# Optimization experiments

Hardware: AMD Instinct MI355X
Metric: run time of the kernel (lower is better)

## Reference

```python
import jax, jax.numpy as jnp
import numpy as np

C = 256
NUM_HEADS = 8
EPS = 1e-5


def setup_inputs() -> dict:
    key = jax.random.key(0)
    ks = jax.random.split(key, 8)
    x = jax.random.normal(ks[0], (2, C, 64, 64), dtype=jnp.float32)
    # LayerNorm params (torch default: weight=1, bias=0)
    norm_w = jnp.ones((C,), jnp.float32)
    norm_b = jnp.zeros((C,), jnp.float32)
    # qkv Linear: weight (3C, C), bias (3C,)
    qkv_w = jax.random.normal(ks[1], (3 * C, C), dtype=jnp.float32) * (1.0 / np.sqrt(C))
    qkv_b = jax.random.normal(ks[2], (3 * C,), dtype=jnp.float32) * 0.01
    # proj Linear: weight (C, C), bias (C,)
    proj_w = jax.random.normal(ks[3], (C, C), dtype=jnp.float32) * (1.0 / np.sqrt(C))
    proj_b = jax.random.normal(ks[4], (C,), dtype=jnp.float32) * 0.01
    # gamma initialized to zeros in torch, but use small nonzero so output depends on attention
    gamma = jnp.full((1,), 0.1, jnp.float32)
    return {"x": x, "norm_w": norm_w, "norm_b": norm_b, "qkv_w": qkv_w,
            "qkv_b": qkv_b, "proj_w": proj_w, "proj_b": proj_b, "gamma": gamma}


def reference(x, norm_w, norm_b, qkv_w, qkv_b, proj_w, proj_b, gamma):
    B, Cc, H, W = x.shape
    N = H * W
    nh = NUM_HEADS
    hd = Cc // nh
    scale = hd ** (-0.5)

    # (B, N, C)
    x_flat = x.reshape(B, Cc, N).transpose(0, 2, 1)

    # LayerNorm over last dim
    mu = jnp.mean(x_flat, axis=-1, keepdims=True)
    var = jnp.mean(jnp.square(x_flat - mu), axis=-1, keepdims=True)
    x_norm = (x_flat - mu) * jax.lax.rsqrt(var + EPS) * norm_w + norm_b

    # QKV projection: (B, N, 3C) -> (3, B, nh, N, hd)
    qkv = x_norm @ qkv_w.T + qkv_b
    qkv = qkv.reshape(B, N, 3, nh, hd).transpose(2, 0, 3, 1, 4)
    q, k, v = qkv[0], qkv[1], qkv[2]

    # attention scores (B, nh, N, N); note torch code scales AFTER q@k.T
    attn = jnp.einsum('bhnd,bhmd->bhnm', q, k) * scale
    attn = jax.nn.softmax(attn, axis=-1)

    # (B, nh, N, hd) -> (B, N, C)
    x_attn = jnp.einsum('bhnm,bhmd->bhnd', attn, v)
    x_attn = x_attn.transpose(0, 2, 1, 3).reshape(B, N, Cc)
    x_attn = x_attn @ proj_w.T + proj_b

    # back to (B, C, H, W) and scaled residual
    x_attn = x_attn.transpose(0, 2, 1).reshape(B, Cc, H, W)
    return gamma * x_attn + x
```

## Files before the change

kernel.cpp:

```cpp
#include <hip/hip_runtime.h>

#define CCH   256
#define NSEQ  4096
#define NH    8
#define HD    32

typedef short s8x __attribute__((ext_vector_type(8)));
typedef float f4x __attribute__((ext_vector_type(4)));

__device__ __forceinline__ f4x mfma16(s8x a, s8x b, f4x c) {
  return __builtin_amdgcn_mfma_f32_16x16x32_bf16(a, b, c, 0, 0, 0);
}

__device__ __forceinline__ unsigned short f2bf(float f) {
  union { float f; unsigned int u; } v; v.f = f;
  unsigned int u = v.u + 0x7fffu + ((v.u >> 16) & 1u);
  return (unsigned short)(u >> 16);
}

__device__ __forceinline__ unsigned int pk_bf_rnd(float lo, float hi) {
  return (unsigned int)f2bf(lo) | ((unsigned int)f2bf(hi) << 16);
}

__device__ __forceinline__ unsigned int pk_bf_trunc(float lo, float hi) {
  union { float f; unsigned int u; } a, b; a.f = lo; b.f = hi;
  return __builtin_amdgcn_perm(b.u, a.u, 0x07060302);
}

#if defined(__has_builtin)
#if __has_builtin(__builtin_amdgcn_exp2f)
#define FEXP2(x) __builtin_amdgcn_exp2f(x)
#endif
#endif
#ifndef FEXP2
__device__ __forceinline__ float __fexp2_asm(float x) {
  float r; asm("v_exp_f32 %0, %1" : "=v"(r) : "v"(x)); return r;
}
#define FEXP2(x) __fexp2_asm(x)
#endif

#define C2SCALE (0.17677669529663689f * 1.4426950408889634f)

__global__ __launch_bounds__(256) void ln_cvt_kernel(const float* __restrict__ x,
                                                     const float* __restrict__ nw,
                                                     const float* __restrict__ nb,
                                                     unsigned short* __restrict__ xn,
                                                     const float* __restrict__ qw,
                                                     const float* __restrict__ pw,
                                                     unsigned short* __restrict__ qwb,
                                                     unsigned short* __restrict__ pwb) {
  if (blockIdx.x >= 256) {
    const int t = (blockIdx.x - 256) * 256 + threadIdx.x;
    const float4* src;
    unsigned short* dst;
    int idx;
    if (t < 49152) { src = reinterpret_cast<const float4*>(qw); dst = qwb; idx = t; }
    else           { src = reinterpret_cast<const float4*>(pw); dst = pwb; idx = t - 49152; }
    const float4 vv = src[idx];
    union { unsigned short u[4]; uint2 v; } pk;
    pk.u[0] = f2bf(vv.x); pk.u[1] = f2bf(vv.y); pk.u[2] = f2bf(vv.z); pk.u[3] = f2bf(vv.w);
    *reinterpret_cast<uint2*>(dst + 4 * idx) = pk.v;
    return;
  }

  __shared__ float Ls[256 * 32];
  __shared__ float Sred[2][32][8];
  const int t  = threadIdx.x;
  const int n  = t & 31;
  const int cg = t >> 5;
  const int p0 = blockIdx.x * 32;
  const int b  = p0 >> 12;
  const int n0 = p0 & 4095;
  const float* xb = x + (size_t)b * CCH * NSEQ + n0;

  #pragma unroll
  for (int i = 0; i < 32; ++i) {
    const int c = i * 8 + cg;
    Ls[c * 32 + (n ^ (c & 31))] = xb[(size_t)c * NSEQ + n];
  }
  __syncthreads();

  float s = 0.f, sq = 0.f;
  #pragma unroll
  for (int j = 0; j < 32; ++j) {
    const int c = cg * 32 + j;
    const float v = Ls[c * 32 + (n ^ j)];
    s += v; sq += v * v;
  }
  Sred[0][n][cg] = s; Sred[1][n][cg] = sq;
  __syncthreads();
  float ts = 0.f, tq = 0.f;
  #pragma unroll
  for (int g = 0; g < 8; ++g) { ts += Sred[0][n][g]; tq += Sred[1][n][g]; }
  const float mean = ts * (1.f / 256.f);
  const float rstd = rsqrtf(tq * (1.f / 256.f) - mean * mean + 1e-5f);

  unsigned short* orow = xn + ((size_t)b * NSEQ + n0 + n) * CCH + cg * 32;
  #pragma unroll
  for (int j8 = 0; j8 < 4; ++j8) {
    unsigned int w_[4];
    #pragma unroll
    for (int hw = 0; hw < 4; ++hw) {
      const int j = j8 * 8 + hw * 2;
      const int c = cg * 32 + j;
      const float v0 = Ls[c * 32 + (n ^ j)];
      const float v1 = Ls[(c + 1) * 32 + (n ^ (j + 1))];
      const float y0 = (v0 - mean) * rstd * nw[c] + nb[c];
      const float y1 = (v1 - mean) * rstd * nw[c + 1] + nb[c + 1];
      w_[hw] = pk_bf_rnd(y0, y1);
    }
    uint4 pkv; pkv.x = w_[0]; pkv.y = w_[1]; pkv.z = w_[2]; pkv.w = w_[3];
    *reinterpret_cast<uint4*>(orow + j8 * 8) = pkv;
  }
}

#define GEMM_CORE(A_PTR, B_PTR, ACC)                                            \
  {                                                                             \
    for (int kb = 0; kb < 4; ++kb) {                                            \
      if (kb) __syncthreads();                                                  \
      _Pragma("unroll")                                                         \
      for (int j = 0; j < 4; ++j) {                                             \
        const int c = j * 256 + tid;                                            \
        const int ar = c >> 3, acr = c & 7;                                     \
        *reinterpret_cast<s8x*>(&As[ar * 64 + ((acr ^ (ar & 7)) << 3)]) =       \
          *reinterpret_cast<const s8x*>(A_PTR + (size_t)(mt * 128 + ar) * CCH + kb * 64 + acr * 8); \
      }                                                                         \
      _Pragma("unroll")                                                         \
      for (int j = 0; j < 2; ++j) {                                             \
        const int c = j * 256 + tid;                                            \
        const int br = c >> 3, bcr = c & 7;                                     \
        *reinterpret_cast<s8x*>(&Bs[br * 64 + ((bcr ^ (br & 7)) << 3)]) =       \
          *reinterpret_cast<const s8x*>(B_PTR + (size_t)(nt * 64 + br) * CCH + kb * 64 + bcr * 8); \
      }                                                                         \
      __syncthreads();                                                          \
      _Pragma("unroll")                                                         \
      for (int kin = 0; kin < 2; ++kin) {                                       \
        const int chx = ((kin * 4 + quad) ^ (l16 & 7)) << 3;                    \
        const s8x a0 = *reinterpret_cast<const s8x*>(&As[(wv * 32 + l16) * 64 + chx]);      \
        const s8x a1 = *reinterpret_cast<const s8x*>(&As[(wv * 32 + 16 + l16) * 64 + chx]); \
        _Pragma("unroll")                                                       \
        for (int ni = 0; ni < 4; ++ni) {                                        \
          const s8x bf = *reinterpret_cast<const s8x*>(&Bs[(ni * 16 + l16) * 64 + chx]);    \
          ACC[0][ni] = mfma16(a0, bf, ACC[0][ni]);                              \
          ACC[1][ni] = mfma16(a1, bf, ACC[1][ni]);                              \
        }                                                                       \
      }                                                                         \
    }                                                                           \
  }

__global__ __launch_bounds__(256, 3) void qkv_gemm(const unsigned short* __restrict__ xn,
                                                   const unsigned short* __restrict__ w,
                                                   const float* __restrict__ bias,
                                                   unsigned short* __restrict__ q,
                                                   unsigned short* __restrict__ k,
                                                   unsigned short* __restrict__ vt) {
  __shared__ unsigned short As[128 * 64];
  __shared__ unsigned short Bs[64 * 64];
  const int tid = threadIdx.x;
  const int wv  = tid >> 6;
  const int lane = tid & 63;
  const int quad = lane >> 4, l16 = lane & 15;
  const int mt = blockIdx.x;
  const int nt = blockIdx.y;

  f4x acc[2][4];
  #pragma unroll
  for (int mi = 0; mi < 2; ++mi)
    #pragma unroll
    for (int ni = 0; ni < 4; ++ni)
      acc[mi][ni] = (f4x){0.f, 0.f, 0.f, 0.f};

  GEMM_CORE(xn, w, acc)

  const int sel = nt >> 2;
  #pragma unroll
  for (int ni = 0; ni < 4; ++ni) {
    const int o = nt * 64 + ni * 16 + l16;
    const float bs = bias[o];
    const int ol = o & 255;
    const int head = ol >> 5, d = ol & 31;
    #pragma unroll
    for (int mi = 0; mi < 2; ++mi) {
      const int g0 = mt * 128 + wv * 32 + mi * 16 + quad * 4;
      const int bb = g0 >> 12, n0 = g0 & 4095;
      if (sel == 2) {
        unsigned short* vp = vt + ((size_t)(bb * NH + head) * HD + d) * NSEQ + n0;
        uint2 pk;
        pk.x = pk_bf_rnd(acc[mi][ni][0] + bs, acc[mi][ni][1] + bs);
        pk.y = pk_bf_rnd(acc[mi][ni][2] + bs, acc[mi][ni][3] + bs);
        *reinterpret_cast<uint2*>(vp) = pk;
      } else {
        const float sc = (sel == 0) ? C2SCALE : 1.f;
        unsigned short* base = (sel == 0) ? q : k;
        #pragma unroll
        for (int r = 0; r < 4; ++r)
          base[((size_t)(bb * NH + head) * NSEQ + n0 + r) * HD + d] = f2bf((acc[mi][ni][r] + bs) * sc);
      }
    }
  }
}

__global__ __launch_bounds__(256, 3) void proj_gemm(const unsigned short* __restrict__ xa,
                                                    const unsigned short* __restrict__ w,
                                                    const float* __restrict__ bias,
                                                    const float* __restrict__ gamma,
                                                    const float* __restrict__ x,
                                                    float* __restrict__ out) {
  __shared__ unsigned short As[128 * 64];
  __shared__ unsigned short Bs[64 * 64];
  const int tid = threadIdx.x;
  const int wv  = tid >> 6;
  const int lane = tid & 63;
  const int quad = lane >> 4, l16 = lane & 15;
  const int mt = blockIdx.x;
  const int nt = blockIdx.y;

  f4x acc[2][4];
  #pragma unroll
  for (int mi = 0; mi < 2; ++mi)
    #pragma unroll
    for (int ni = 0; ni < 4; ++ni)
      acc[mi][ni] = (f4x){0.f, 0.f, 0.f, 0.f};

  GEMM_CORE(xa, w, acc)

  const float g0 = gamma[0];
  #pragma unroll
  for (int ni = 0; ni < 4; ++ni) {
    const int c = nt * 64 + ni * 16 + l16;
    const float bs = bias[c];
    #pragma unroll
    for (int mi = 0; mi < 2; ++mi) {
      const int gr = mt * 128 + wv * 32 + mi * 16 + quad * 4;
      const int bb = gr >> 12, n0 = gr & 4095;
      const size_t off = (size_t)(bb * CCH + c) * NSEQ + n0;
      const float4 xv = *reinterpret_cast<const float4*>(x + off);
      float4 ov;
      ov.x = g0 * (acc[mi][ni][0] + bs) + xv.x;
      ov.y = g0 * (acc[mi][ni][1] + bs) + xv.y;
      ov.z = g0 * (acc[mi][ni][2] + bs) + xv.z;
      ov.w = g0 * (acc[mi][ni][3] + bs) + xv.w;
      *reinterpret_cast<float4*>(out + off) = ov;
    }
  }
}

__global__ __launch_bounds__(256, 4) void fa_kernel(const unsigned short* __restrict__ q,
                                                    const unsigned short* __restrict__ k,
                                                    const unsigned short* __restrict__ vt,
                                                    float* __restrict__ Opart,
                                                    float* __restrict__ Lpart) {
  __shared__ unsigned short Ks[2][64 * 40];
  __shared__ unsigned short Vs[2][32 * 72];
  __shared__ unsigned short Ps[128 * 72];

  const int tid  = threadIdx.x;
  const int wv   = tid >> 6;
  const int lane = tid & 63;
  const int quad = lane >> 4;
  const int l16  = lane & 15;
  const int i    = blockIdx.x;
  const int bh   = i & 15;
  const int rest = i >> 4;
  const int half = rest & 1;
  const int qblk = rest >> 1;
  const int kv0  = half * 2048;

  const unsigned short* kb_ = k  + ((size_t)bh * NSEQ + kv0) * HD;
  const unsigned short* vb_ = vt + (size_t)bh * HD * NSEQ + kv0;

  const int krow = tid >> 2;
  const int kdc  = (tid & 3) * 8;
  const int vrow = tid >> 3;
  const int vkc  = (tid & 7) * 8;

  s8x bq0, bq1;
  {
    const unsigned short* qb = q + ((size_t)bh * NSEQ + (size_t)qblk * 128 + wv * 32) * HD;
    bq0 = *reinterpret_cast<const s8x*>(qb + (size_t)l16 * HD + quad * 8);
    bq1 = *reinterpret_cast<const s8x*>(qb + (size_t)(16 + l16) * HD + quad * 8);
  }

  uint4 kreg = *reinterpret_cast<const uint4*>(kb_ + (size_t)krow * HD + kdc);
  uint4 vreg = *reinterpret_cast<const uint4*>(vb_ + (size_t)vrow * NSEQ + vkc);
  *reinterpret_cast<uint4*>(&Ks[0][krow * 40 + kdc]) = kreg;
  *reinterpret_cast<uint4*>(&Vs[0][vrow * 72 + vkc]) = vreg;
  kreg = *reinterpret_cast<const uint4*>(kb_ + (size_t)(64 + krow) * HD + kdc);
  vreg = *reinterpret_cast<const uint4*>(vb_ + (size_t)vrow * NSEQ + 64 + vkc);
  __syncthreads();

  f4x st[4][2];
  #pragma unroll
  for (int ii = 0; ii < 4; ++ii) {
    const s8x ak = *reinterpret_cast<const s8x*>(&Ks[0][(ii * 16 + l16) * 40 + quad * 8]);
    const f4x z = {0.f, 0.f, 0.f, 0.f};
    st[ii][0] = mfma16(ak, bq0, z);
    st[ii][1] = mfma16(ak, bq1, z);
  }

  f4x oacc[2][2];
  #pragma unroll
  for (int dt = 0; dt < 2; ++dt)
    #pragma unroll
    for (int ct = 0; ct < 2; ++ct)
      oacc[dt][ct] = (f4x){0.f, 0.f, 0.f, 0.f};
  f4x accL[2] = {(f4x){0.f, 0.f, 0.f, 0.f}, (f4x){0.f, 0.f, 0.f, 0.f}};

  s8x ones;
  #pragma unroll
  for (int j = 0; j < 8; ++j) ones[j] = (short)0x3F80;

  const int r0 = (wv * 32 + l16) * 72;
  const int r1 = (wv * 32 + 16 + l16) * 72;

  for (int t = 0; t < 32; ++t) {
    const int c = t & 1;

    if (t + 1 < 32) {
      *reinterpret_cast<uint4*>(&Ks[c ^ 1][krow * 40 + kdc]) = kreg;
      *reinterpret_cast<uint4*>(&Vs[c ^ 1][vrow * 72 + vkc]) = vreg;
    }

    #pragma unroll
    for (int ct = 0; ct < 2; ++ct) {
      const int prow = (wv * 32 + ct * 16 + l16) * 72;
      #pragma unroll
      for (int ii = 0; ii < 4; ++ii) {
        const float e0 = FEXP2(st[ii][ct][0]);
        const float e1 = FEXP2(st[ii][ct][1]);
        const float e2 = FEXP2(st[ii][ct][2]);
        const float e3 = FEXP2(st[ii][ct][3]);
        uint2 pw;
        pw.x = pk_bf_trunc(e0, e1);
        pw.y = pk_bf_trunc(e2, e3);
        *reinterpret_cast<uint2*>(&Ps[prow + ii * 16 + quad * 4]) = pw;
      }
    }

    if (t + 2 < 32) {
      kreg = *reinterpret_cast<const uint4*>(kb_ + (size_t)((t + 2) * 64 + krow) * HD + kdc);
      vreg = *reinterpret_cast<const uint4*>(vb_ + (size_t)vrow * NSEQ + (t + 2) * 64 + vkc);
    }

    #pragma unroll
    for (int kb2 = 0; kb2 < 2; ++kb2) {
      const s8x bp0 = *reinterpret_cast<const s8x*>(&Ps[r0 + kb2 * 32 + quad * 8]);
      const s8x bp1 = *reinterpret_cast<const s8x*>(&Ps[r1 + kb2 * 32 + quad * 8]);
      const s8x av0 = *reinterpret_cast<const s8x*>(&Vs[c][l16 * 72 + kb2 * 32 + quad * 8]);
      const s8x av1 = *reinterpret_cast<const s8x*>(&Vs[c][(16 + l16) * 72 + kb2 * 32 + quad * 8]);
      oacc[0][0] = mfma16(av0, bp0, oacc[0][0]);
      oacc[1][0] = mfma16(av1, bp0, oacc[1][0]);
      oacc[0][1] = mfma16(av0, bp1, oacc[0][1]);
      oacc[1][1] = mfma16(av1, bp1, oacc[1][1]);
      accL[0] = mfma16(ones, bp0, accL[0]);
      accL[1] = mfma16(ones, bp1, accL[1]);
    }

    __syncthreads();

    if (t + 1 < 32) {
      #pragma unroll
      for (int ii = 0; ii < 4; ++ii) {
        const s8x ak = *reinterpret_cast<const s8x*>(&Ks[c ^ 1][(ii * 16 + l16) * 40 + quad * 8]);
        const f4x z = {0.f, 0.f, 0.f, 0.f};
        st[ii][0] = mfma16(ak, bq0, z);
        st[ii][1] = mfma16(ak, bq1, z);
      }
    }
  }

  #pragma unroll
  for (int ct = 0; ct < 2; ++ct) {
    const int qg = qblk * 128 + wv * 32 + ct * 16 + l16;
    float* obase = Opart + ((size_t)(half * 16 + bh) * NSEQ + qg) * HD;
    #pragma unroll
    for (int dt = 0; dt < 2; ++dt) {
      float4 ov;
      ov.x = oacc[dt][ct][0]; ov.y = oacc[dt][ct][1];
      ov.z = oacc[dt][ct][2]; ov.w = oacc[dt][ct][3];
      *reinterpret_cast<float4*>(obase + dt * 16 + quad * 4) = ov;
    }
    if (quad == 0)
      Lpart[(size_t)(half * 16 + bh) * NSEQ + qg] = accL[ct][0];
  }
}

__global__ __launch_bounds__(256) void fa_combine(const float* __restrict__ Opart,
                                                  const float* __restrict__ Lpart,
                                                  unsigned short* __restrict__ xa) {
  const int t  = blockIdx.x * 256 + threadIdx.x;
  const int c8 = t & 3;
  const int n  = (t >> 2) & 4095;
  const int bh = t >> 14;
  const int b  = bh >> 3, h = bh & 7;

  const size_t o0 = ((size_t)bh * NSEQ + n) * HD + c8 * 8;
  const size_t o1 = o0 + (size_t)16 * NSEQ * HD;
  const float4 a0 = *reinterpret_cast<const float4*>(Opart + o0);
  const float4 a1 = *reinterpret_cast<const float4*>(Opart + o0 + 4);
  const float4 b0 = *reinterpret_cast<const float4*>(Opart + o1);
  const float4 b1 = *reinterpret_cast<const float4*>(Opart + o1 + 4);
  const float l0 = Lpart[(size_t)bh * NSEQ + n];
  const float l1 = Lpart[(size_t)(16 + bh) * NSEQ + n];
  const float rl = 1.f / (l0 + l1);

  uint4 ow;
  ow.x = pk_bf_rnd((a0.x + b0.x) * rl, (a0.y + b0.y) * rl);
  ow.y = pk_bf_rnd((a0.z + b0.z) * rl, (a0.w + b0.w) * rl);
  ow.z = pk_bf_rnd((a1.x + b1.x) * rl, (a1.y + b1.y) * rl);
  ow.w = pk_bf_rnd((a1.z + b1.z) * rl, (a1.w + b1.w) * rl);
  *reinterpret_cast<uint4*>(xa + ((size_t)b * NSEQ + n) * CCH + h * HD + c8 * 8) = ow;
}

extern "C" void kernel_launch(void* const* d_in, const int* in_sizes, int n_in,
                              void* d_out, int out_size, void* d_ws, size_t ws_size,
                              hipStream_t stream) {
  const float* x      = (const float*)d_in[0];
  const float* norm_w = (const float*)d_in[1];
  const float* norm_b = (const float*)d_in[2];
  const float* qkv_w  = (const float*)d_in[3];
  const float* qkv_b  = (const float*)d_in[4];
  const float* proj_w = (const float*)d_in[5];
  const float* proj_b = (const float*)d_in[6];
  const float* gamma  = (const float*)d_in[7];
  float* out = (float*)d_out;

  char* ws = (char*)d_ws;
  unsigned short* xn  = (unsigned short*)(ws);
  unsigned short* qwb = (unsigned short*)(ws + 4194304);
  unsigned short* pwb = (unsigned short*)(ws + 4587520);
  unsigned short* q   = (unsigned short*)(ws + 4718592);
  unsigned short* k   = (unsigned short*)(ws + 8912896);
  unsigned short* vt  = (unsigned short*)(ws + 13107200);
  unsigned short* xa  = (unsigned short*)(ws + 17301504);
  float* Opart        = (float*)(ws + 21495808);
  float* Lpart        = (float*)(ws + 38273024);

  hipLaunchKernelGGL(ln_cvt_kernel, dim3(512), dim3(256), 0, stream,
                     x, norm_w, norm_b, xn, qkv_w, proj_w, qwb, pwb);
  hipLaunchKernelGGL(qkv_gemm,  dim3(64, 12), dim3(256), 0, stream, xn, qwb, qkv_b, q, k, vt);
  hipLaunchKernelGGL(fa_kernel, dim3(1024), dim3(256), 0, stream, q, k, vt, Opart, Lpart);
  hipLaunchKernelGGL(fa_combine, dim3(1024), dim3(256), 0, stream, Opart, Lpart, xa);
  hipLaunchKernelGGL(proj_gemm, dim3(64, 4), dim3(256), 0, stream, xa, pwb, proj_b, gamma, x, out);
}
```

Measured before the change: 154.8 us.

## Load K/V straight into registers and software-pipeline PV with double-buffered P

Each wave now loads its K and V MFMA fragments directly from global memory into double-buffered registers, instead of staging them through shared memory. This removes the shared K/V tiles and the per-iteration __syncthreads. The P·V product is deferred by one iteration, using a double-buffered P tile in LDS that each wave owns privately, so the exp/pack work overlaps the MFMA work. In exchange, every wave re-reads the full K/V tile, which raises global and L2 traffic roughly fourfold, and register pressure rises enough that launch bounds drop from 4 to 3 blocks per CU.

```diff
diff --git a/kernel.cpp b/kernel.cpp
--- a/kernel.cpp
+++ b/kernel.cpp
@@ -245,14 +245,12 @@
   }
 }
 
-__global__ __launch_bounds__(256, 4) void fa_kernel(const unsigned short* __restrict__ q,
+__global__ __launch_bounds__(256, 3) void fa_kernel(const unsigned short* __restrict__ q,
                                                     const unsigned short* __restrict__ k,
                                                     const unsigned short* __restrict__ vt,
                                                     float* __restrict__ Opart,
                                                     float* __restrict__ Lpart) {
-  __shared__ unsigned short Ks[2][64 * 40];
-  __shared__ unsigned short Vs[2][32 * 72];
-  __shared__ unsigned short Ps[128 * 72];
+  __shared__ unsigned short Ps[2][128 * 72];
 
   const int tid  = threadIdx.x;
   const int wv   = tid >> 6;
@@ -269,10 +267,9 @@
   const unsigned short* kb_ = k  + ((size_t)bh * NSEQ + kv0) * HD;
   const unsigned short* vb_ = vt + (size_t)bh * HD * NSEQ + kv0;
 
-  const int krow = tid >> 2;
-  const int kdc  = (tid & 3) * 8;
-  const int vrow = tid >> 3;
-  const int vkc  = (tid & 7) * 8;
+  const unsigned short* kp  = kb_ + (size_t)l16 * HD + quad * 8;
+  const unsigned short* vpA = vb_ + (size_t)l16 * NSEQ + quad * 8;
+  const unsigned short* vpB = vb_ + (size_t)(16 + l16) * NSEQ + quad * 8;
 
   s8x bq0, bq1;
   {
@@ -281,21 +278,25 @@
     bq1 = *reinterpret_cast<const s8x*>(qb + (size_t)(16 + l16) * HD + quad * 8);
   }
 
-  uint4 kreg = *reinterpret_cast<const uint4*>(kb_ + (size_t)krow * HD + kdc);
-  uint4 vreg = *reinterpret_cast<const uint4*>(vb_ + (size_t)vrow * NSEQ + vkc);
-  *reinterpret_cast<uint4*>(&Ks[0][krow * 40 + kdc]) = kreg;
-  *reinterpret_cast<uint4*>(&Vs[0][vrow * 72 + vkc]) = vreg;
-  kreg = *reinterpret_cast<const uint4*>(kb_ + (size_t)(64 + krow) * HD + kdc);
-  vreg = *reinterpret_cast<const uint4*>(vb_ + (size_t)vrow * NSEQ + 64 + vkc);
-  __syncthreads();
+  s8x akA[4], akB[4], avA[4], avB[4];
+  #pragma unroll
+  for (int ii = 0; ii < 4; ++ii)
+    akA[ii] = *reinterpret_cast<const s8x*>(kp + ii * 16 * HD);
+  #pragma unroll
+  for (int kb2 = 0; kb2 < 2; ++kb2) {
+    avA[kb2]     = *reinterpret_cast<const s8x*>(vpA + kb2 * 32);
+    avA[2 + kb2] = *reinterpret_cast<const s8x*>(vpB + kb2 * 32);
+  }
+  #pragma unroll
+  for (int ii = 0; ii < 4; ++ii)
+    akB[ii] = *reinterpret_cast<const s8x*>(kp + (64 + ii * 16) * HD);
 
   f4x st[4][2];
   #pragma unroll
   for (int ii = 0; ii < 4; ++ii) {
-    const s8x ak = *reinterpret_cast<const s8x*>(&Ks[0][(ii * 16 + l16) * 40 + quad * 8]);
     const f4x z = {0.f, 0.f, 0.f, 0.f};
-    st[ii][0] = mfma16(ak, bq0, z);
-    st[ii][1] = mfma16(ak, bq1, z);
+    st[ii][0] = mfma16(akA[ii], bq0, z);
+    st[ii][1] = mfma16(akA[ii], bq1, z);
   }
 
   f4x oacc[2][2];
@@ -311,61 +312,88 @@
   for (int j = 0; j < 8; ++j) ones[j] = (short)0x3F80;
 
   const int r0 = (wv * 32 + l16) * 72;
-  const int r1 = (wv * 32 + 16 + l16) * 72;
-
-  for (int t = 0; t < 32; ++t) {
-    const int c = t & 1;
-
-    if (t + 1 < 32) {
-      *reinterpret_cast<uint4*>(&Ks[c ^ 1][krow * 40 + kdc]) = kreg;
-      *reinterpret_cast<uint4*>(&Vs[c ^ 1][vrow * 72 + vkc]) = vreg;
-    }
-
-    #pragma unroll
-    for (int ct = 0; ct < 2; ++ct) {
-      const int prow = (wv * 32 + ct * 16 + l16) * 72;
-      #pragma unroll
-      for (int ii = 0; ii < 4; ++ii) {
-        const float e0 = FEXP2(st[ii][ct][0]);
-        const float e1 = FEXP2(st[ii][ct][1]);
-        const float e2 = FEXP2(st[ii][ct][2]);
-        const float e3 = FEXP2(st[ii][ct][3]);
-        uint2 pw;
-        pw.x = pk_bf_trunc(e0, e1);
-        pw.y = pk_bf_trunc(e2, e3);
-        *reinterpret_cast<uint2*>(&Ps[prow + ii * 16 + quad * 4]) = pw;
-      }
-    }
-
-    if (t + 2 < 32) {
-      kreg = *reinterpret_cast<const uint4*>(kb_ + (size_t)((t + 2) * 64 + krow) * HD + kdc);
-      vreg = *reinterpret_cast<const uint4*>(vb_ + (size_t)vrow * NSEQ + (t + 2) * 64 + vkc);
-    }
-
+  const int r1 = r0 + 16 * 72;
+
+  #define FA_ITER(T, AKN, AKS, AVP)                                             \
+  {                                                                             \
+    const int t_ = (T);                                                         \
+        \
+    if (t_ > 0) {                                                               \
+      const unsigned short* pb = Ps[(t_ - 1) & 1];                              \
+      _Pragma("unroll")                                                         \
+      for (int kb2 = 0; kb2 < 2; ++kb2) {                                       \
+        const s8x bp0 = *reinterpret_cast<const s8x*>(&pb[r0 + kb2 * 32 + quad * 8]); \
+        const s8x bp1 = *reinterpret_cast<const s8x*>(&pb[r1 + kb2 * 32 + quad * 8]); \
+        oacc[0][0] = mfma16(AVP[kb2],     bp0, oacc[0][0]);                     \
+        oacc[1][0] = mfma16(AVP[2 + kb2], bp0, oacc[1][0]);                     \
+        oacc[0][1] = mfma16(AVP[kb2],     bp1, oacc[0][1]);                     \
+        oacc[1][1] = mfma16(AVP[2 + kb2], bp1, oacc[1][1]);                     \
+        accL[0] = mfma16(ones, bp0, accL[0]);                                   \
+        accL[1] = mfma16(ones, bp1, accL[1]);                                   \
+      }                                                                         \
+    }                                                                           \
+                           \
+    {                                                                           \
+      unsigned short* pdst = Ps[t_ & 1];                                        \
+      _Pragma("unroll")                                                         \
+      for (int ct = 0; ct < 2; ++ct) {                                          \
+        const int prow = r0 + ct * 16 * 72;                                     \
+        _Pragma("unroll")                                                       \
+        for (int ii = 0; ii < 4; ++ii) {                                        \
+          const float e0 = FEXP2(st[ii][ct][0]);                                \
+          const float e1 = FEXP2(st[ii][ct][1]);                                \
+          const float e2 = FEXP2(st[ii][ct][2]);                                \
+          const float e3 = FEXP2(st[ii][ct][3]);                                \
+          uint2 pw;                                                             \
+          pw.x = pk_bf_trunc(e0, e1);                                           \
+          pw.y = pk_bf_trunc(e2, e3);                                           \
+          *reinterpret_cast<uint2*>(&pdst[prow + ii * 16 + quad * 4]) = pw;     \
+        }                                                                       \
+      }                                                                         \
+    }                                                                           \
+          \
+    if (t_ + 2 < 32) {                                                          \
+      const unsigned short* kn = kp + (size_t)(t_ + 2) * 64 * HD;               \
+      _Pragma("unroll")                                                         \
+      for (int ii = 0; ii < 4; ++ii)                                            \
+        AKN[ii] = *reinterpret_cast<const s8x*>(kn + ii * 16 * HD);             \
+    }                                                                           \
+    if (t_ + 1 < 32) {                                                          \
+      _Pragma("unroll")                                                         \
+      for (int kb2 = 0; kb2 < 2; ++kb2) {                                       \
+        AVP[kb2]     = *reinterpret_cast<const s8x*>(vpA + (t_ + 1) * 64 + kb2 * 32); \
+        AVP[2 + kb2] = *reinterpret_cast<const s8x*>(vpB + (t_ + 1) * 64 + kb2 * 32); \
+      }                                                                         \
+    }                                                                           \
+           \
+    if (t_ + 1 < 32) {                                                          \
+      _Pragma("unroll")                                                         \
+      for (int ii = 0; ii < 4; ++ii) {                                          \
+        const f4x z = {0.f, 0.f, 0.f, 0.f};                                     \
+        st[ii][0] = mfma16(AKS[ii], bq0, z);                                    \
+        st[ii][1] = mfma16(AKS[ii], bq1, z);                                    \
+      }                                                                         \
+    }                                                                           \
+  }
+
+  for (int t = 0; t < 32; t += 2) {
+    FA_ITER(t,     akA, akB, avB)
+    FA_ITER(t + 1, akB, akA, avA)
+  }
+  #undef FA_ITER
+
+  {
+    const unsigned short* pb = Ps[1];
     #pragma unroll
     for (int kb2 = 0; kb2 < 2; ++kb2) {
-      const s8x bp0 = *reinterpret_cast<const s8x*>(&Ps[r0 + kb2 * 32 + quad * 8]);
-      const s8x bp1 = *reinterpret_cast<const s8x*>(&Ps[r1 + kb2 * 32 + quad * 8]);
-      const s8x av0 = *reinterpret_cast<const s8x*>(&Vs[c][l16 * 72 + kb2 * 32 + quad * 8]);
-      const s8x av1 = *reinterpret_cast<const s8x*>(&Vs[c][(16 + l16) * 72 + kb2 * 32 + quad * 8]);
-      oacc[0][0] = mfma16(av0, bp0, oacc[0][0]);
-      oacc[1][0] = mfma16(av1, bp0, oacc[1][0]);
-      oacc[0][1] = mfma16(av0, bp1, oacc[0][1]);
-      oacc[1][1] = mfma16(av1, bp1, oacc[1][1]);
+      const s8x bp0 = *reinterpret_cast<const s8x*>(&pb[r0 + kb2 * 32 + quad * 8]);
+      const s8x bp1 = *reinterpret_cast<const s8x*>(&pb[r1 + kb2 * 32 + quad * 8]);
+      oacc[0][0] = mfma16(avB[kb2],     bp0, oacc[0][0]);
+      oacc[1][0] = mfma16(avB[2 + kb2], bp0, oacc[1][0]);
+      oacc[0][1] = mfma16(avB[kb2],     bp1, oacc[0][1]);
+      oacc[1][1] = mfma16(avB[2 + kb2], bp1, oacc[1][1]);
       accL[0] = mfma16(ones, bp0, accL[0]);
       accL[1] = mfma16(ones, bp1, accL[1]);
-    }
-
-    __syncthreads();
-
-    if (t + 1 < 32) {
-      #pragma unroll
-      for (int ii = 0; ii < 4; ++ii) {
-        const s8x ak = *reinterpret_cast<const s8x*>(&Ks[c ^ 1][(ii * 16 + l16) * 40 + quad * 8]);
-        const f4x z = {0.f, 0.f, 0.f, 0.f};
-        st[ii][0] = mfma16(ak, bq0, z);
-        st[ii][1] = mfma16(ak, bq1, z);
-      }
     }
   }
 
```

Measured after the change: 187.7 us. 1.21x slower.
